# Optimization experiments

Measured on AMD Instinct MI355X. Metric: run time of the kernel, lower is better.

## Reference

```python
import jax, jax.numpy as jnp
import numpy as np

N = 768  # length of time vector

def setup_inputs() -> dict:
    key = jax.random.key(0)
    ks = jax.random.split(key, 4)
    # time vector (sorted grid-like values, as in a GP time axis)
    x = jnp.sort(jax.random.uniform(ks[0], (N,), dtype=jnp.float32) * (6 * np.pi))
    # MLP params: Linear(2,1024) -> Sigmoid -> Linear(1024,128) -> ReLU -> Linear(128,1)
    W1 = jax.random.normal(ks[1], (1024, 2), dtype=jnp.float32) * (1.0 / np.sqrt(2.0))
    b1 = jnp.zeros((1024,), dtype=jnp.float32)
    W2 = jax.random.normal(ks[2], (128, 1024), dtype=jnp.float32) * (1.0 / np.sqrt(1024.0))
    b2 = jnp.zeros((128,), dtype=jnp.float32)
    W3 = jax.random.normal(ks[3], (1, 128), dtype=jnp.float32) * (1.0 / np.sqrt(128.0))
    b3 = jnp.zeros((1,), dtype=jnp.float32)
    return {"x": x, "W1": W1, "b1": b1, "W2": W2, "b2": b2, "W3": W3, "b3": b3}


def reference(x, W1, b1, W2, b2, W3, b3):
    n = x.shape[0]
    # all (i, j) with j >= i  -> n(n+1)/2 pairs; replaces the Python double loop
    iu, ju = jnp.triu_indices(n)
    pairs = jnp.stack([x[iu], x[ju]], axis=-1)            # [P, 2]
    h = jax.nn.sigmoid(pairs @ W1.T + b1)                 # [P, 1024]
    h = jax.nn.relu(h @ W2.T + b2)                        # [P, 128]
    v = (h @ W3.T + b3)[:, 0]                             # [P]
    # K starts as eye; upper triangle INCLUDING diagonal is overwritten
    K = jnp.eye(n, dtype=x.dtype).at[iu, ju].set(v)       # [n, n] upper-triangular
    return K.T @ K                                        # symmetric PSD covariance
```

## Files before the change

### kernel.cpp

```cpp
#include <hip/hip_runtime.h>
#include <hip/hip_bf16.h>

#define NN 768
#define MD 1024
#define NPAIR 295296
#define NPBLK2 2307

typedef __attribute__((ext_vector_type(8))) short s16x8;
typedef __attribute__((ext_vector_type(4))) float f32x4;
typedef __attribute__((ext_vector_type(2))) float f32x2;
typedef __attribute__((ext_vector_type(2))) __bf16 b16x2;

__device__ __forceinline__ ushort bf16_rn(float f) {
    uint u = __builtin_bit_cast(uint, f);
    u += 0x7FFFu + ((u >> 16) & 1u);
    return (ushort)(u >> 16);
}

__device__ __forceinline__ void ptoij(int p, int& io, int& jo) {
    const float disc = (float)(1537 * 1537 - 8 * p);
    int i = (int)((1537.0f - sqrtf(disc)) * 0.5f);
    i = i < 0 ? 0 : (i > 767 ? 767 : i);
    while (i > 0 && p < i * (1537 - i) / 2) --i;
    while (i < 767 && p >= (i + 1) * (1536 - i) / 2) ++i;
    io = i;
    jo = i + (p - i * (1537 - i) / 2);
}

__global__ __launch_bounds__(256) void w2frag(const float* __restrict__ W2,
                                              ushort* __restrict__ WF)
{
    const int id = blockIdx.x * 256 + threadIdx.x;
    const int lane = id & 63;
    const int f = id >> 6;
    const int tn = f & 7;
    const int ks = (f >> 3) & 1;
    const int c  = f >> 4;
    const int k = tn * 16 + (lane & 15);
    const int m = c * 64 + ks * 32 + (lane >> 4) * 8;
    const float4 a = *reinterpret_cast<const float4*>(W2 + k * MD + m);
    const float4 b = *reinterpret_cast<const float4*>(W2 + k * MD + m + 4);
    const float w[8] = {a.x, a.y, a.z, a.w, b.x, b.y, b.z, b.w};
    s16x8 h;
#pragma unroll
    for (int e = 0; e < 8; ++e) h[e] = (short)bf16_rn(w[e]);
    *reinterpret_cast<s16x8*>(WF + id * 8) = h;
}

#define LOADB(cc, ks)                                                        \
    {                                                                        \
        const ushort* wb_ = WF + (cc) * 8192 + (ks) * 4096 + lane * 8;       \
        _Pragma("unroll")                                                    \
        for (int tn_ = 0; tn_ < 8; ++tn_)                                    \
            bh[tn_] = *reinterpret_cast<const s16x8*>(wb_ + tn_ * 512);      \
    }

#define SIG_HALF(cc, ks_)                                                    \
    {                                                                        \
        const int m0_ = (cc) * 64 + (ks_) * 32 + l4 * 8;                     \
        const f32x4 a0_ = *reinterpret_cast<const f32x4*>(&sa[m0_]);         \
        const f32x4 a1_ = *reinterpret_cast<const f32x4*>(&sa[m0_ + 4]);     \
        const f32x4 c0_ = *reinterpret_cast<const f32x4*>(&sc[m0_]);         \
        const f32x4 c1_ = *reinterpret_cast<const f32x4*>(&sc[m0_ + 4]);     \
        const f32x4 b0_ = *reinterpret_cast<const f32x4*>(&sb[m0_]);         \
        const f32x4 b1_ = *reinterpret_cast<const f32x4*>(&sb[m0_ + 4]);     \
        _Pragma("unroll")                                                    \
        for (int tm_ = 0; tm_ < 2; ++tm_) {                                  \
            const f32x2 xi2_ = (f32x2){xia[tm_], xia[tm_]};                  \
            const f32x2 xj2_ = (f32x2){xja[tm_], xja[tm_]};                  \
            const f32x2 one2_ = (f32x2){1.f, 1.f};                           \
            union { s16x8 v; uint u[4]; } fr_;                               \
            _Pragma("unroll")                                                \
            for (int h_ = 0; h_ < 4; ++h_) {                                 \
                f32x2 av_, cv_, bv_;                                         \
                if (h_ < 2) {                                                \
                    av_ = (f32x2){a0_[2 * h_], a0_[2 * h_ + 1]};             \
                    cv_ = (f32x2){c0_[2 * h_], c0_[2 * h_ + 1]};             \
                    bv_ = (f32x2){b0_[2 * h_], b0_[2 * h_ + 1]};             \
                } else {                                                     \
                    av_ = (f32x2){a1_[2 * h_ - 4], a1_[2 * h_ - 3]};         \
                    cv_ = (f32x2){c1_[2 * h_ - 4], c1_[2 * h_ - 3]};         \
                    bv_ = (f32x2){b1_[2 * h_ - 4], b1_[2 * h_ - 3]};         \
                }                                                            \
                const f32x2 u2_ = __builtin_elementwise_fma(                 \
                    xi2_, av_, __builtin_elementwise_fma(xj2_, cv_, bv_));   \
                f32x2 e2_;                                                   \
                e2_[0] = __builtin_amdgcn_exp2f(u2_[0]);                     \
                e2_[1] = __builtin_amdgcn_exp2f(u2_[1]);                     \
                const f32x2 t2_ = e2_ + one2_;                               \
                b16x2 p_;                                                    \
                p_.x = (__bf16)__builtin_amdgcn_rcpf(t2_[0]);                \
                p_.y = (__bf16)__builtin_amdgcn_rcpf(t2_[1]);                \
                fr_.u[h_] = __builtin_bit_cast(uint, p_);                    \
            }                                                                \
            ah[tm_] = fr_.v;                                                 \
        }                                                                    \
    }

#define MFMA_HALF()                                                          \
    {                                                                        \
        __builtin_amdgcn_s_setprio(1);                                       \
        _Pragma("unroll")                                                    \
        for (int tm_ = 0; tm_ < 2; ++tm_)                                    \
            _Pragma("unroll")                                                \
            for (int tn_ = 0; tn_ < 8; ++tn_)                                \
                acc[tm_][tn_] = __builtin_amdgcn_mfma_f32_16x16x32_bf16(     \
                    ah[tm_], bh[tn_], acc[tm_][tn_], 0, 0, 0);               \
        __builtin_amdgcn_s_setprio(0);                                       \
    }

__global__ __launch_bounds__(256, 3) void mlp_pairs_reg(
    const float* __restrict__ x,
    const float* __restrict__ W1, const float* __restrict__ b1,
    const ushort* __restrict__ WF,
    const float* __restrict__ b2, const float* __restrict__ W3,
    const float* __restrict__ b3, float* __restrict__ K)
{
    __shared__ __align__(16) float sa[MD], sc[MD], sb[MD];

    const int t = threadIdx.x;
    const int lane = t & 63;
    const int l15 = lane & 15, l4 = lane >> 4;
    const int wv = t >> 6;

    const float NL2E = -1.4426950408889634f;
    for (int m = t; m < MD; m += 256) {
        const float2 w = reinterpret_cast<const float2*>(W1)[m];
        sa[m] = w.x * NL2E;
        sc[m] = w.y * NL2E;
        sb[m] = b1[m] * NL2E;
    }

    const int pairbase = blockIdx.x * 128 + wv * 32;

    float xia[2], xja[2];
#pragma unroll
    for (int tm = 0; tm < 2; ++tm) {
        const int p = pairbase + tm * 16 + l15;
        if (p < NPAIR) {
            int i, j;
            ptoij(p, i, j);
            xia[tm] = x[i];
            xja[tm] = x[j];
        } else {
            xia[tm] = 0.f;
            xja[tm] = 0.f;
        }
    }

    f32x4 acc[2][8];
#pragma unroll
    for (int a = 0; a < 2; ++a)
#pragma unroll
        for (int b = 0; b < 8; ++b) acc[a][b] = (f32x4){0.f, 0.f, 0.f, 0.f};

    s16x8 bh[8];
    LOADB(0, 0);
    __syncthreads();

    s16x8 ah[2];
    for (int c = 0; c < 16; ++c) {
        SIG_HALF(c, 0);
        MFMA_HALF();
        LOADB(c, 1);
        SIG_HALF(c, 1);
        MFMA_HALF();
        if (c < 15) LOADB(c + 1, 0);
    }

    float w3v[8], b2v[8];
#pragma unroll
    for (int tn = 0; tn < 8; ++tn) {
        const int k = tn * 16 + l15;
        w3v[tn] = W3[k];
        b2v[tn] = b2[k];
    }
    const float b3v = b3[0];
#pragma unroll
    for (int tm = 0; tm < 2; ++tm)
#pragma unroll
        for (int r = 0; r < 4; ++r) {
            float v = 0.f;
#pragma unroll
            for (int tn = 0; tn < 8; ++tn)
                v = fmaf(w3v[tn], fmaxf(acc[tm][tn][r] + b2v[tn], 0.f), v);
            v += __shfl_xor(v, 1, 16);
            v += __shfl_xor(v, 2, 16);
            v += __shfl_xor(v, 4, 16);
            v += __shfl_xor(v, 8, 16);
            if (l15 == 0) {
                const int p = pairbase + tm * 16 + l4 * 4 + r;
                if (p < NPAIR) {
                    int i, j;
                    ptoij(p, i, j);
                    K[i * NN + j] = v + b3v;
                }
            }
        }
}

#define MC 32
#define JT 128
#define SPAD 132
__global__ __launch_bounds__(256) void mlp_fill(
    const float* __restrict__ x,
    const float* __restrict__ W1, const float* __restrict__ b1,
    const float* __restrict__ W2, const float* __restrict__ b2,
    const float* __restrict__ W3, const float* __restrict__ b3,
    float* __restrict__ K)
{
    const int i  = blockIdx.y;
    const int j0 = blockIdx.x * JT;
    if (j0 + JT - 1 < i) return;
    __shared__ float sA[MD];
    __shared__ float sCw[MD];
    __shared__ float sxj[JT];
    __shared__ float S[MC][SPAD];
    __shared__ float W2t[MC][SPAD];
    const int t = threadIdx.x;
    const float xi = x[i];
    for (int m = t; m < MD; m += 256) {
        const float2 w = reinterpret_cast<const float2*>(W1)[m];
        sA[m]  = fmaf(xi, w.x, b1[m]);
        sCw[m] = w.y;
    }
    if (t < JT) sxj[t] = x[j0 + t];
    const int tk = t & 15;
    const int tj = t >> 4;
    float w3r[8], b2r[8];
#pragma unroll
    for (int kk = 0; kk < 8; kk++) {
        w3r[kk] = W3[tk * 8 + kk];
        b2r[kk] = b2[tk * 8 + kk];
    }
    float acc[8][8];
#pragma unroll
    for (int jj = 0; jj < 8; jj++)
#pragma unroll
        for (int kk = 0; kk < 8; kk++) acc[jj][kk] = 0.f;
    const int jx   = t & 127;
    const int mseg = (t >> 7) * 16;
    __syncthreads();
    const float xjv = sxj[jx];
    for (int m0 = 0; m0 < MD; m0 += MC) {
#pragma unroll
        for (int q = 0; q < 4; q++) {
            const int f   = t + q * 256;
            const int k   = f >> 3;
            const int mm4 = (f & 7) * 4;
            const float4 w = *reinterpret_cast<const float4*>(W2 + k * MD + m0 + mm4);
            W2t[mm4 + 0][k] = w.x;
            W2t[mm4 + 1][k] = w.y;
            W2t[mm4 + 2][k] = w.z;
            W2t[mm4 + 3][k] = w.w;
        }
#pragma unroll
        for (int q = 0; q < 16; q++) {
            const int ml = mseg + q;
            const float z = fmaf(xjv, sCw[m0 + ml], sA[m0 + ml]);
            S[ml][jx] = 1.0f / (1.0f + __expf(-z));
        }
        __syncthreads();
#pragma unroll 4
        for (int mm = 0; mm < MC; mm++) {
            const float4 s0 = *reinterpret_cast<const float4*>(&S[mm][tj * 8]);
            const float4 s1 = *reinterpret_cast<const float4*>(&S[mm][tj * 8 + 4]);
            const float4 w0 = *reinterpret_cast<const float4*>(&W2t[mm][tk * 8]);
            const float4 w1 = *reinterpret_cast<const float4*>(&W2t[mm][tk * 8 + 4]);
            const float sj[8] = {s0.x, s0.y, s0.z, s0.w, s1.x, s1.y, s1.z, s1.w};
            const float wk[8] = {w0.x, w0.y, w0.z, w0.w, w1.x, w1.y, w1.z, w1.w};
#pragma unroll
            for (int jj = 0; jj < 8; jj++)
#pragma unroll
                for (int kk = 0; kk < 8; kk++)
                    acc[jj][kk] = fmaf(sj[jj], wk[kk], acc[jj][kk]);
        }
        __syncthreads();
    }
    const float b3v = b3[0];
#pragma unroll
    for (int jj = 0; jj < 8; jj++) {
        float v = 0.f;
#pragma unroll
        for (int kk = 0; kk < 8; kk++) {
            const float h = acc[jj][kk] + b2r[kk];
            v = fmaf(w3r[kk], fmaxf(h, 0.f), v);
        }
#pragma unroll
        for (int off = 8; off >= 1; off >>= 1)
            v += __shfl_xor(v, off, 16);
        if (tk == 0) {
            const int j = j0 + tj * 8 + jj;
            if (j >= i) K[i * NN + j] = v + b3v;
        }
    }
}

__global__ __launch_bounds__(256) void ktk(const float* __restrict__ K,
                                           float* __restrict__ C)
{
    const int b0 = blockIdx.x * 64;
    const int a0 = blockIdx.y * 64;
    if (b0 < a0) return;
    __shared__ float Ka[64][68];
    __shared__ float Kb[64][68];
    const int t  = threadIdx.x;
    const int tb = t & 15;
    const int ta = t >> 4;
    float acc[4][4];
#pragma unroll
    for (int u = 0; u < 4; u++)
#pragma unroll
        for (int v = 0; v < 4; v++) acc[u][v] = 0.f;
    const int kmax = a0 + 64;
    for (int k0 = 0; k0 < kmax; k0 += 64) {
#pragma unroll
        for (int q = 0; q < 4; q++) {
            const int f  = t + q * 256;
            const int kk = f >> 4;
            const int c4 = (f & 15) * 4;
            *reinterpret_cast<float4*>(&Ka[kk][c4]) =
                *reinterpret_cast<const float4*>(K + (k0 + kk) * NN + a0 + c4);
            *reinterpret_cast<float4*>(&Kb[kk][c4]) =
                *reinterpret_cast<const float4*>(K + (k0 + kk) * NN + b0 + c4);
        }
        __syncthreads();
#pragma unroll 8
        for (int kk = 0; kk < 64; kk++) {
            const float4 av = *reinterpret_cast<const float4*>(&Ka[kk][ta * 4]);
            const float4 bv = *reinterpret_cast<const float4*>(&Kb[kk][tb * 4]);
            const float a4[4] = {av.x, av.y, av.z, av.w};
            const float b4[4] = {bv.x, bv.y, bv.z, bv.w};
#pragma unroll
            for (int u = 0; u < 4; u++)
#pragma unroll
                for (int v = 0; v < 4; v++)
                    acc[u][v] = fmaf(a4[u], b4[v], acc[u][v]);
        }
        __syncthreads();
    }
#pragma unroll
    for (int u = 0; u < 4; u++) {
        float4 o;
        o.x = acc[u][0]; o.y = acc[u][1]; o.z = acc[u][2]; o.w = acc[u][3];
        *reinterpret_cast<float4*>(C + (a0 + ta * 4 + u) * NN + b0 + tb * 4) = o;
    }
    if (b0 > a0) {
#pragma unroll
        for (int v = 0; v < 4; v++) {
            float4 o;
            o.x = acc[0][v]; o.y = acc[1][v]; o.z = acc[2][v]; o.w = acc[3][v];
            *reinterpret_cast<float4*>(C + (b0 + tb * 4 + v) * NN + a0 + ta * 4) = o;
        }
    }
}

extern "C" void kernel_launch(void* const* d_in, const int* in_sizes, int n_in,
                              void* d_out, int out_size, void* d_ws, size_t ws_size,
                              hipStream_t stream)
{
    const float* x  = (const float*)d_in[0];
    const float* W1 = (const float*)d_in[1];
    const float* b1 = (const float*)d_in[2];
    const float* W2 = (const float*)d_in[3];
    const float* b2 = (const float*)d_in[4];
    const float* W3 = (const float*)d_in[5];
    const float* b3 = (const float*)d_in[6];
    float* Kmat = (float*)d_ws;
    float* C    = (float*)d_out;

    const size_t kBytes = (size_t)NN * NN * sizeof(float);
    const size_t need   = kBytes + 262144;

    hipMemsetAsync(Kmat, 0, kBytes, stream);
    if (ws_size >= need) {
        ushort* WF = (ushort*)((char*)d_ws + kBytes);
        w2frag<<<64, 256, 0, stream>>>(W2, WF);
        mlp_pairs_reg<<<NPBLK2, 256, 0, stream>>>(x, W1, b1, WF, b2, W3, b3, Kmat);
    } else {
        mlp_fill<<<dim3(6, NN), 256, 0, stream>>>(x, W1, b1, W2, b2, W3, b3, Kmat);
    }
    ktk<<<dim3(NN / 64, NN / 64), 256, 0, stream>>>(Kmat, C);
}
```

Baseline: 166.1 us.

## Factor sigmoid exponent into precomputed per-row and per-column exp tables

Splits the sigmoid argument exp(-(a_i + c*x_j)) into a product of two precomputed exponentials: a per-row fp32 table and a per-column bf16 table already laid out in MFMA fragment order. The MLP kernel then computes each sigmoid with one FMA and one reciprocal instead of an exp, and is tiled per (i, 128-j) block with the row table loaded into LDS via global_load_lds. The aim is to remove the transcendental cost from the hot loop and the per-pair index decoding. In exchange it adds two prep kernels and extra workspace, loses some precision because the column exponential is rounded to bf16 and can overflow for large arguments, and drops the old fallback path when workspace is small.

```diff
diff --git a/kernel.cpp b/kernel.cpp
--- a/kernel.cpp
+++ b/kernel.cpp
@@ -26,6 +26,11 @@
     io = i;
     jo = i + (p - i * (1537 - i) / 2);
 }
+
+#define GLOAD16(gsrc, ldst)                                                        \
+    __builtin_amdgcn_global_load_lds(                                              \
+        (const __attribute__((address_space(1))) void*)(gsrc),                     \
+        (__attribute__((address_space(3))) void*)(ldst), 16, 0, 0)
 
 __global__ __launch_bounds__(256) void w2frag(const float* __restrict__ W2,
                                               ushort* __restrict__ WF)
@@ -45,6 +50,169 @@
 #pragma unroll
     for (int e = 0; e < 8; ++e) h[e] = (short)bf16_rn(w[e]);
     *reinterpret_cast<s16x8*>(WF + id * 8) = h;
+}
+
+__global__ __launch_bounds__(256) void eaprep(const float* __restrict__ x,
+                                              const float* __restrict__ W1,
+                                              const float* __restrict__ b1,
+                                              float* __restrict__ EAg)
+{
+    const int i = blockIdx.x;
+    const float xi = x[i];
+    const float NL2E = -1.4426950408889634f;
+    for (int m = threadIdx.x; m < MD; m += 256) {
+        const float2 w = reinterpret_cast<const float2*>(W1)[m];
+        EAg[i * MD + m] = __builtin_amdgcn_exp2f(fmaf(w.x, xi, b1[m]) * NL2E);
+    }
+}
+
+__global__ __launch_bounds__(256) void ecfprep(const float* __restrict__ x,
+                                               const float* __restrict__ W1,
+                                               ushort* __restrict__ ECF)
+{
+    const int id = blockIdx.x * 256 + threadIdx.x;
+    const int j = id >> 7;
+    const int m8 = id & 127;
+    const float xj = x[j];
+    const float NL2E = -1.4426950408889634f;
+    const int mbase = m8 * 8;
+    s16x8 h;
+#pragma unroll
+    for (int e = 0; e < 8; ++e) {
+        const float cm = W1[(mbase + e) * 2 + 1];
+        h[e] = (short)bf16_rn(__builtin_amdgcn_exp2f(cm * xj * NL2E));
+    }
+    const int c    = mbase >> 6;
+    const int ks   = (mbase >> 5) & 1;
+    const int l4   = (mbase & 31) >> 3;
+    const int lane = l4 * 16 + (j & 15);
+    const int off  = (j >> 4) * 16384 + c * 1024 + ks * 512 + lane * 8;
+    *reinterpret_cast<s16x8*>(ECF + off) = h;
+}
+
+#define LOADB_T(cc, ks)                                                      \
+    {                                                                        \
+        const ushort* wb_ = WF + (cc) * 8192 + (ks) * 4096 + lane * 8;       \
+        _Pragma("unroll")                                                    \
+        for (int tn_ = 0; tn_ < 8; ++tn_)                                    \
+            bh[tn_] = *reinterpret_cast<const s16x8*>(wb_ + tn_ * 512);      \
+    }
+
+#define LOADEC(cc, ks, dst)                                                  \
+    {                                                                        \
+        const ushort* e_ = ECF + jg0 * 16384 + (cc) * 1024 + (ks) * 512 + lane * 8; \
+        dst[0] = *reinterpret_cast<const s16x8*>(e_);                        \
+        dst[1] = *reinterpret_cast<const s16x8*>(e_ + 16384);                \
+    }
+
+#define SIG_T(cc, ks_, ec)                                                   \
+    {                                                                        \
+        const int m0_ = (cc) * 64 + (ks_) * 32 + l4 * 8;                     \
+        const f32x4 ea0_ = *reinterpret_cast<const f32x4*>(&EAl[m0_]);       \
+        const f32x4 ea1_ = *reinterpret_cast<const f32x4*>(&EAl[m0_ + 4]);   \
+        _Pragma("unroll")                                                    \
+        for (int tm_ = 0; tm_ < 2; ++tm_) {                                  \
+            union { s16x8 v; uint u[4]; } ec_;                               \
+            ec_.v = ec[tm_];                                                 \
+            union { s16x8 v; uint u[4]; } fr_;                               \
+            _Pragma("unroll")                                                \
+            for (int h_ = 0; h_ < 4; ++h_) {                                 \
+                const uint uu_ = ec_.u[h_];                                  \
+                const float el_ = __builtin_bit_cast(float, uu_ << 16);      \
+                const float eh_ = __builtin_bit_cast(float, uu_ & 0xFFFF0000u); \
+                const float ga_ = (h_ < 2) ? ea0_[2 * h_] : ea1_[2 * h_ - 4];     \
+                const float gb_ = (h_ < 2) ? ea0_[2 * h_ + 1] : ea1_[2 * h_ - 3]; \
+                const float t0_ = fmaf(el_, ga_, 1.0f);                      \
+                const float t1_ = fmaf(eh_, gb_, 1.0f);                      \
+                b16x2 p_;                                                    \
+                p_.x = (__bf16)__builtin_amdgcn_rcpf(t0_);                   \
+                p_.y = (__bf16)__builtin_amdgcn_rcpf(t1_);                   \
+                fr_.u[h_] = __builtin_bit_cast(uint, p_);                    \
+            }                                                                \
+            ah[tm_] = fr_.v;                                                 \
+        }                                                                    \
+    }
+
+#define MFMA_T()                                                             \
+    {                                                                        \
+        __builtin_amdgcn_s_setprio(1);                                       \
+        _Pragma("unroll")                                                    \
+        for (int tm_ = 0; tm_ < 2; ++tm_)                                    \
+            _Pragma("unroll")                                                \
+            for (int tn_ = 0; tn_ < 8; ++tn_)                                \
+                acc[tm_][tn_] = __builtin_amdgcn_mfma_f32_16x16x32_bf16(     \
+                    ah[tm_], bh[tn_], acc[tm_][tn_], 0, 0, 0);               \
+        __builtin_amdgcn_s_setprio(0);                                       \
+    }
+
+__global__ __launch_bounds__(256, 3) void mlp_tab(
+    const float* __restrict__ EAg, const ushort* __restrict__ ECF,
+    const ushort* __restrict__ WF,
+    const float* __restrict__ b2, const float* __restrict__ W3,
+    const float* __restrict__ b3, float* __restrict__ K)
+{
+    const int i  = blockIdx.y;
+    const int j0 = blockIdx.x * 128;
+    if (j0 + 127 < i) return;
+
+    __shared__ __align__(16) float EAl[MD];
+
+    const int t = threadIdx.x;
+    const int lane = t & 63, wv = t >> 6;
+    const int l15 = lane & 15, l4 = lane >> 4;
+
+    const int jw  = j0 + wv * 32;
+    const int jg0 = jw >> 4;
+
+    GLOAD16(EAg + i * MD + wv * 256 + lane * 4, (char*)EAl + wv * 1024);
+
+    f32x4 acc[2][8];
+#pragma unroll
+    for (int a = 0; a < 2; ++a)
+#pragma unroll
+        for (int b = 0; b < 8; ++b) acc[a][b] = (f32x4){0.f, 0.f, 0.f, 0.f};
+
+    s16x8 bh[8], ecA[2], ecB[2], ah[2];
+    LOADB_T(0, 0);
+    LOADEC(0, 0, ecA);
+    __syncthreads();
+
+    for (int c = 0; c < 16; ++c) {
+        LOADEC(c, 1, ecB);
+        SIG_T(c, 0, ecA);
+        MFMA_T();
+        LOADB_T(c, 1);
+        if (c < 15) LOADEC(c + 1, 0, ecA);
+        SIG_T(c, 1, ecB);
+        MFMA_T();
+        if (c < 15) LOADB_T(c + 1, 0);
+    }
+
+    float w3v[8], b2v[8];
+#pragma unroll
+    for (int tn = 0; tn < 8; ++tn) {
+        const int k = tn * 16 + l15;
+        w3v[tn] = W3[k];
+        b2v[tn] = b2[k];
+    }
+    const float b3v = b3[0];
+#pragma unroll
+    for (int tm = 0; tm < 2; ++tm)
+#pragma unroll
+        for (int r = 0; r < 4; ++r) {
+            float v = 0.f;
+#pragma unroll
+            for (int tn = 0; tn < 8; ++tn)
+                v = fmaf(w3v[tn], fmaxf(acc[tm][tn][r] + b2v[tn], 0.f), v);
+            v += __shfl_xor(v, 1, 16);
+            v += __shfl_xor(v, 2, 16);
+            v += __shfl_xor(v, 4, 16);
+            v += __shfl_xor(v, 8, 16);
+            if (l15 == 0) {
+                const int j = jw + tm * 16 + l4 * 4 + r;
+                if (j >= i) K[i * NN + j] = v + b3v;
+            }
+        }
 }
 
 #define LOADB(cc, ks)                                                        \
@@ -199,103 +367,6 @@
         }
 }
 
-#define MC 32
-#define JT 128
-#define SPAD 132
-__global__ __launch_bounds__(256) void mlp_fill(
-    const float* __restrict__ x,
-    const float* __restrict__ W1, const float* __restrict__ b1,
-    const float* __restrict__ W2, const float* __restrict__ b2,
-    const float* __restrict__ W3, const float* __restrict__ b3,
-    float* __restrict__ K)
-{
-    const int i  = blockIdx.y;
-    const int j0 = blockIdx.x * JT;
-    if (j0 + JT - 1 < i) return;
-    __shared__ float sA[MD];
-    __shared__ float sCw[MD];
-    __shared__ float sxj[JT];
-    __shared__ float S[MC][SPAD];
-    __shared__ float W2t[MC][SPAD];
-    const int t = threadIdx.x;
-    const float xi = x[i];
-    for (int m = t; m < MD; m += 256) {
-        const float2 w = reinterpret_cast<const float2*>(W1)[m];
-        sA[m]  = fmaf(xi, w.x, b1[m]);
-        sCw[m] = w.y;
-    }
-    if (t < JT) sxj[t] = x[j0 + t];
-    const int tk = t & 15;
-    const int tj = t >> 4;
-    float w3r[8], b2r[8];
-#pragma unroll
-    for (int kk = 0; kk < 8; kk++) {
-        w3r[kk] = W3[tk * 8 + kk];
-        b2r[kk] = b2[tk * 8 + kk];
-    }
-    float acc[8][8];
-#pragma unroll
-    for (int jj = 0; jj < 8; jj++)
-#pragma unroll
-        for (int kk = 0; kk < 8; kk++) acc[jj][kk] = 0.f;
-    const int jx   = t & 127;
-    const int mseg = (t >> 7) * 16;
-    __syncthreads();
-    const float xjv = sxj[jx];
-    for (int m0 = 0; m0 < MD; m0 += MC) {
-#pragma unroll
-        for (int q = 0; q < 4; q++) {
-            const int f   = t + q * 256;
-            const int k   = f >> 3;
-            const int mm4 = (f & 7) * 4;
-            const float4 w = *reinterpret_cast<const float4*>(W2 + k * MD + m0 + mm4);
-            W2t[mm4 + 0][k] = w.x;
-            W2t[mm4 + 1][k] = w.y;
-            W2t[mm4 + 2][k] = w.z;
-            W2t[mm4 + 3][k] = w.w;
-        }
-#pragma unroll
-        for (int q = 0; q < 16; q++) {
-            const int ml = mseg + q;
-            const float z = fmaf(xjv, sCw[m0 + ml], sA[m0 + ml]);
-            S[ml][jx] = 1.0f / (1.0f + __expf(-z));
-        }
-        __syncthreads();
-#pragma unroll 4
-        for (int mm = 0; mm < MC; mm++) {
-            const float4 s0 = *reinterpret_cast<const float4*>(&S[mm][tj * 8]);
-            const float4 s1 = *reinterpret_cast<const float4*>(&S[mm][tj * 8 + 4]);
-            const float4 w0 = *reinterpret_cast<const float4*>(&W2t[mm][tk * 8]);
-            const float4 w1 = *reinterpret_cast<const float4*>(&W2t[mm][tk * 8 + 4]);
-            const float sj[8] = {s0.x, s0.y, s0.z, s0.w, s1.x, s1.y, s1.z, s1.w};
-            const float wk[8] = {w0.x, w0.y, w0.z, w0.w, w1.x, w1.y, w1.z, w1.w};
-#pragma unroll
-            for (int jj = 0; jj < 8; jj++)
-#pragma unroll
-                for (int kk = 0; kk < 8; kk++)
-                    acc[jj][kk] = fmaf(sj[jj], wk[kk], acc[jj][kk]);
-        }
-        __syncthreads();
-    }
-    const float b3v = b3[0];
-#pragma unroll
-    for (int jj = 0; jj < 8; jj++) {
-        float v = 0.f;
-#pragma unroll
-        for (int kk = 0; kk < 8; kk++) {
-            const float h = acc[jj][kk] + b2r[kk];
-            v = fmaf(w3r[kk], fmaxf(h, 0.f), v);
-        }
-#pragma unroll
-        for (int off = 8; off >= 1; off >>= 1)
-            v += __shfl_xor(v, off, 16);
-        if (tk == 0) {
-            const int j = j0 + tj * 8 + jj;
-            if (j >= i) K[i * NN + j] = v + b3v;
-        }
-    }
-}
-
 __global__ __launch_bounds__(256) void ktk(const float* __restrict__ K,
                                            float* __restrict__ C)
 {
@@ -369,16 +440,26 @@
     float* Kmat = (float*)d_ws;
     float* C    = (float*)d_out;
 
-    const size_t kBytes = (size_t)NN * NN * sizeof(float);
-    const size_t need   = kBytes + 262144;
+    const size_t kBytes  = (size_t)NN * NN * sizeof(float);
+    const size_t wBytes  = 262144;
+    const size_t eaB     = (size_t)NN * MD * sizeof(float);
+    const size_t ecB     = (size_t)48 * 16384 * sizeof(ushort);
+    const size_t needTab = kBytes + wBytes + eaB + ecB;
+    const size_t needFB  = kBytes + wBytes;
 
     hipMemsetAsync(Kmat, 0, kBytes, stream);
-    if (ws_size >= need) {
+    if (ws_size >= needTab) {
+        ushort* WF  = (ushort*)((char*)d_ws + kBytes);
+        float*  EAg = (float*)((char*)d_ws + kBytes + wBytes);
+        ushort* ECF = (ushort*)((char*)d_ws + kBytes + wBytes + eaB);
+        w2frag<<<64, 256, 0, stream>>>(W2, WF);
+        eaprep<<<NN, 256, 0, stream>>>(x, W1, b1, EAg);
+        ecfprep<<<384, 256, 0, stream>>>(x, W1, ECF);
+        mlp_tab<<<dim3(6, NN), 256, 0, stream>>>(EAg, ECF, WF, b2, W3, b3, Kmat);
+    } else if (ws_size >= needFB) {
         ushort* WF = (ushort*)((char*)d_ws + kBytes);
         w2frag<<<64, 256, 0, stream>>>(W2, WF);
         mlp_pairs_reg<<<NPBLK2, 256, 0, stream>>>(x, W1, b1, WF, b2, W3, b3, Kmat);
-    } else {
-        mlp_fill<<<dim3(6, NN), 256, 0, stream>>>(x, W1, b1, W2, b2, W3, b3, Kmat);
     }
     ktk<<<dim3(NN / 64, NN / 64), 256, 0, stream>>>(Kmat, C);
 }
```

Result: slower. 179.9 us (+8.3%).
